# Kernel optimization log

Hardware: AMD Instinct MI355X
Metric: run time of the kernel (lower is better)

Reference implementation:

```python
import jax, jax.numpy as jnp
import numpy as np

B, P, N, E, H, D = 8, 1000, 1000, 128, 8, 16  # batch, pomo, nodes, embed, heads, qkv_dim
SQRT_E = float(np.sqrt(E))
CLIP = 10.0
INV_SQRT_D = 1.0 / float(np.sqrt(D))


def _heads(x):
    # [b, n, H*D] -> [b, H, n, D]
    b, n, _ = x.shape
    return x.reshape(b, n, H, D).transpose(0, 2, 1, 3)


def _mha(q, k, v, ninf_mask):
    # q: [b,H,P,D], k/v: [b,H,N,D], ninf_mask: [b,P,N]
    score = jnp.einsum('bhnd,bhsd->bhns', q, k) * INV_SQRT_D
    score = score + ninf_mask[:, None, :, :]
    w = jax.nn.softmax(score, axis=-1)
    out = jnp.einsum('bhns,bhsd->bhnd', w, v)
    return out.transpose(0, 2, 1, 3).reshape(q.shape[0], q.shape[2], H * D)


def setup_inputs() -> dict:
    key = jax.random.key(0)
    ks = jax.random.split(key, 16)
    s = 0.02
    return {
        'encoded_last_node': jax.random.normal(ks[0], (B, P, E), jnp.float32),
        'attr': jax.random.normal(ks[1], (B, P, 4), jnp.float32),
        'encoded_nodes': jax.random.normal(ks[2], (B, N, E), jnp.float32),
        'ninf_mask': jnp.zeros((B, P, N), jnp.float32),
        'Wq_shared': jax.random.normal(ks[3], (E + 4, H * D), jnp.float32) * s,
        'Wk_shared': jax.random.normal(ks[4], (E, H * D), jnp.float32) * s,
        'Wv_shared': jax.random.normal(ks[5], (E, H * D), jnp.float32) * s,
        'Wq_task': jax.random.normal(ks[6], (E + 4, H * D), jnp.float32) * s,
        'Wk_task': jax.random.normal(ks[7], (E, H * D), jnp.float32) * s,
        'Wv_task': jax.random.normal(ks[8], (E, H * D), jnp.float32) * s,
        'Wc_shared': jax.random.normal(ks[9], (H * D, E), jnp.float32) * s,
        'bc_shared': jnp.zeros((E,), jnp.float32),
        'Wc_task': jax.random.normal(ks[10], (H * D, E), jnp.float32) * s,
        'bc_task': jnp.zeros((E,), jnp.float32),
        'Wg': jax.random.normal(ks[11], (E + 4, E), jnp.float32) * s,
        'bg': jnp.zeros((E,), jnp.float32),
    }


def reference(encoded_last_node, attr, encoded_nodes, ninf_mask,
              Wq_shared, Wk_shared, Wv_shared, Wq_task, Wk_task, Wv_task,
              Wc_shared, bc_shared, Wc_task, bc_task, Wg, bg):
    # set_kv
    k_shared = _heads(encoded_nodes @ Wk_shared)
    v_shared = _heads(encoded_nodes @ Wv_shared)
    k_task = _heads(encoded_nodes @ Wk_task)
    v_task = _heads(encoded_nodes @ Wv_task)

    # decoder forward
    input_cat = jnp.concatenate([encoded_last_node, attr], axis=2)  # [B,P,E+4]
    q_shared = _heads(input_cat @ Wq_shared)
    q_task = _heads(input_cat @ Wq_task)

    out_shared = _mha(q_shared, k_shared, v_shared, ninf_mask) @ Wc_shared + bc_shared
    out_task = _mha(q_task, k_task, v_task, ninf_mask) @ Wc_task + bc_task

    gate = jax.nn.sigmoid(input_cat @ Wg + bg)
    gated_out = gate * out_shared + (1.0 - gate) * out_task  # [B,P,E]

    # pointer scores against single-head key (encoded_nodes)
    score = jnp.einsum('bpe,bne->bpn', gated_out, encoded_nodes) / SQRT_E
    score_clipped = CLIP * jnp.tanh(score)
    probs = jax.nn.softmax(score_clipped + ninf_mask, axis=2)
    return probs
```

## Files before the change

kernel.cpp:

```cpp
#include <hip/hip_runtime.h>
#include <math.h>

#define BB 8
#define PP 1000
#define NN 1000
#define EE 128
#define HH 8
#define DD 16

#define INV_SQRT_E 0.08838834764831845f
#define LOG2E      1.4426950408889634f
#define QSCALE     0.3606737602222409f

typedef short short8_t __attribute__((ext_vector_type(8)));
typedef float f32x4    __attribute__((ext_vector_type(4)));
typedef float f32x16   __attribute__((ext_vector_type(16)));
typedef __bf16 bf16x4  __attribute__((ext_vector_type(4)));
typedef __bf16 bf16x8  __attribute__((ext_vector_type(8)));

__device__ __forceinline__ float sigmoid_fast(float x) {
    return 1.f / (1.f + __expf(-x));
}
__device__ __forceinline__ float tanh_fast(float x) {
    x = fminf(fmaxf(x, -15.f), 15.f);
    float e = __expf(2.f * x);
    return (e - 1.f) / (e + 1.f);
}

__device__ __forceinline__ f32x4 mfma16(short8_t a, short8_t b, f32x4 c) {
    return __builtin_amdgcn_mfma_f32_16x16x32_bf16(a, b, c, 0, 0, 0);
}
__device__ __forceinline__ f32x16 mfma32(short8_t a, short8_t b, f32x16 c) {
    return __builtin_amdgcn_mfma_f32_32x32x16_bf16(a, b, c, 0, 0, 0);
}

__device__ __forceinline__ float sum16(float x) {
    int v;
    v = __builtin_amdgcn_update_dpp(0, __builtin_bit_cast(int, x), 0xB1, 0xF, 0xF, true);
    x += __builtin_bit_cast(float, v);
    v = __builtin_amdgcn_update_dpp(0, __builtin_bit_cast(int, x), 0x4E, 0xF, 0xF, true);
    x += __builtin_bit_cast(float, v);
    v = __builtin_amdgcn_update_dpp(0, __builtin_bit_cast(int, x), 0x141, 0xF, 0xF, true);
    x += __builtin_bit_cast(float, v);
    v = __builtin_amdgcn_update_dpp(0, __builtin_bit_cast(int, x), 0x140, 0xF, 0xF, true);
    x += __builtin_bit_cast(float, v);
    return x;
}

__global__ __launch_bounds__(256) void prep_kernel(
    const float* __restrict__ mask, const float* __restrict__ nodes,
    const float* __restrict__ eln,  const float* __restrict__ attr,
    const float* __restrict__ Wk_s, const float* __restrict__ Wv_s,
    const float* __restrict__ Wk_t, const float* __restrict__ Wv_t,
    const float* __restrict__ Wq_s, const float* __restrict__ Wq_t,
    const float* __restrict__ Wg,   const float* __restrict__ Wc_s,
    const float* __restrict__ Wc_t,
    __bf16* __restrict__ emaskb, __bf16* __restrict__ nodesb,
    __bf16* __restrict__ inb, __bf16* __restrict__ Wtb)
{
    const int bx = blockIdx.x;
    __shared__ float tile[32][129];
    if (bx < 7813) {
        int i = (bx * 256 + threadIdx.x) * 4;
        if (i < 8000000) {
            float4 v = *(const float4*)&mask[i];
            bf16x4 pk = { (__bf16)(v.x * LOG2E), (__bf16)(v.y * LOG2E),
                          (__bf16)(v.z * LOG2E), (__bf16)(v.w * LOG2E) };
            *(bf16x4*)&emaskb[i] = pk;
        }
    } else if (bx < 8813) {
        int i = ((bx - 7813) * 256 + threadIdx.x) * 4;
        float4 v = *(const float4*)&nodes[i];
        bf16x4 pk = { (__bf16)v.x, (__bf16)v.y, (__bf16)v.z, (__bf16)v.w };
        *(bf16x4*)&nodesb[i] = pk;
    } else if (bx < 9438) {
        int t = (bx - 8813) * 256 + threadIdx.x;
        int row = t / 20, seg = t - row * 20;
        bf16x8 o = {};
        if (seg < 16) {
            const float* p = &eln[(size_t)row * 128 + seg * 8];
            float4 a = *(const float4*)p, b = *(const float4*)(p + 4);
            o = bf16x8{ (__bf16)a.x, (__bf16)a.y, (__bf16)a.z, (__bf16)a.w,
                        (__bf16)b.x, (__bf16)b.y, (__bf16)b.z, (__bf16)b.w };
        } else if (seg == 16) {
            float4 a = *(const float4*)&attr[(size_t)row * 4];
            o = bf16x8{ (__bf16)a.x, (__bf16)a.y, (__bf16)a.z, (__bf16)a.w,
                        (__bf16)0.f, (__bf16)0.f, (__bf16)0.f, (__bf16)0.f };
        }
        *(bf16x8*)&inb[(size_t)row * 160 + seg * 8] = o;
    } else {
        int idx = bx - 9438;
        int m = idx / 5, kt = idx - m * 5;
        const float* srcs[9] = {Wk_s, Wv_s, Wk_t, Wv_t, Wq_s, Wq_t, Wg, Wc_s, Wc_t};
        const int   srcKs[9] = {128, 128, 128, 128, 132, 132, 132, 128, 128};
        const int   kpads[9] = {128, 128, 128, 128, 160, 160, 160, 128, 128};
        const size_t offs[9] = {0, 16384, 32768, 49152, 65536, 86016, 106496, 126976, 143360};
        const int kp = kpads[m];
        if (kt * 32 >= kp) return;
        const float* src = srcs[m];
        const int sK = srcKs[m];
        const size_t off = offs[m];
        const int tid = threadIdx.x;
        for (int j = tid; j < 32 * 128; j += 256) {
            int kk = j >> 7, n = j & 127;
            int k = kt * 32 + kk;
            tile[kk][n] = (k < sK) ? src[(size_t)k * 128 + n] : 0.f;
        }
        __syncthreads();
        for (int j = tid; j < 32 * 128; j += 256) {
            int n = j >> 5, kk = j & 31;
            Wtb[off + (size_t)n * kp + kt * 32 + kk] = (__bf16)tile[kk][n];
        }
    }
}

template<int NC>
__device__ __forceinline__ void proj_body(
    const __bf16* __restrict__ A, const __bf16* __restrict__ W,
    f32x4 acc[8], int r0, int quad, int lq)
{
    const int K = NC * 32;
    short8_t aF[NC];
    #pragma unroll
    for (int c = 0; c < NC; ++c)
        aF[c] = *(const short8_t*)&A[(size_t)(r0 + lq) * K + c * 32 + quad * 8];
    #pragma unroll
    for (int nt = 0; nt < 8; ++nt) {
        acc[nt] = f32x4{0.f, 0.f, 0.f, 0.f};
        #pragma unroll
        for (int c = 0; c < NC; ++c) {
            short8_t bF = *(const short8_t*)&W[(size_t)(nt * 16 + lq) * K + c * 32 + quad * 8];
            acc[nt] = mfma16(aF[c], bF, acc[nt]);
        }
    }
}

__global__ __launch_bounds__(256) void proj_mfma_kernel(
    const __bf16* __restrict__ nodesb, const __bf16* __restrict__ inb,
    const __bf16* __restrict__ Wtb,
    __bf16* __restrict__ kb_s, __bf16* __restrict__ vt_s,
    __bf16* __restrict__ kb_t, __bf16* __restrict__ vt_t,
    __bf16* __restrict__ qb_s, __bf16* __restrict__ qb_t)
{
    const int wsel = blockIdx.y;
    const int wave = threadIdx.x >> 6, lane = threadIdx.x & 63;
    const int quad = lane >> 4, lq = lane & 15;
    const int r0 = blockIdx.x * 64 + wave * 16;

    f32x4 acc[8];
    if (wsel < 4) {
        proj_body<4>(nodesb, Wtb + (size_t)wsel * 16384, acc, r0, quad, lq);
    } else {
        proj_body<5>(inb, Wtb + 65536 + (size_t)(wsel - 4) * 20480, acc, r0, quad, lq);
    }

    if (wsel == 0 || wsel == 2) {
        __bf16* O = (wsel == 0) ? kb_s : kb_t;
        #pragma unroll
        for (int r = 0; r < 4; ++r) {
            int m = r0 + quad * 4 + r;
            int b = m / 1000, n = m - b * 1000;
            #pragma unroll
            for (int nt = 0; nt < 8; ++nt)
                O[(((size_t)(b * 8 + nt) * 1000 + n) << 4) + lq] = (__bf16)acc[nt][r];
        }
    } else if (wsel == 4 || wsel == 5) {
        __bf16* O = (wsel == 4) ? qb_s : qb_t;
        #pragma unroll
        for (int r = 0; r < 4; ++r) {
            int m = r0 + quad * 4 + r;
            int b = m / 1000, n = m - b * 1000;
            #pragma unroll
            for (int nt = 0; nt < 8; ++nt)
                O[(((size_t)(b * 8 + nt) * 1000 + n) << 4) + lq] =
                    (__bf16)(acc[nt][r] * QSCALE);
        }
    } else {
        __bf16* O = (wsel == 1) ? vt_s : vt_t;
        #pragma unroll
        for (int r = 0; r < 4; ++r) {
            int m = r0 + quad * 4 + r;
            int b = m / 1000, n = m - b * 1000;
            int rr = n & 31;
            int pos = (n & ~31) + ((rr < 16) ? (rr << 1) : (((rr - 16) << 1) | 1));
            #pragma unroll
            for (int nt = 0; nt < 8; ++nt)
                O[(((size_t)(b * 8 + nt) * 16 + lq) << 10) + pos] = (__bf16)acc[nt][r];
        }
    }
}

__global__ __launch_bounds__(256) void attn_mfma_kernel(
    const __bf16* __restrict__ qb_s, const __bf16* __restrict__ qb_t,
    const __bf16* __restrict__ kb_s, const __bf16* __restrict__ kb_t,
    const __bf16* __restrict__ vt_s, const __bf16* __restrict__ vt_t,
    const __bf16* __restrict__ emaskb,
    __bf16* __restrict__ att_s, __bf16* __restrict__ att_t)
{
    const int b    = blockIdx.z;
    const int wave = threadIdx.x >> 6;
    const int combo = blockIdx.y * 4 + wave;
    const int br = combo & 1;
    const int h  = combo >> 1;
    const __bf16* Q  = br ? qb_t : qb_s;
    const __bf16* K  = br ? kb_t : kb_s;
    const __bf16* Vt = br ? vt_t : vt_s;
    __bf16* O        = br ? att_t : att_s;
    const int lane = threadIdx.x & 63;
    const int quad = lane >> 4, lq = lane & 15;
    const int col  = lane & 31;
    const int half = lane >> 5;
    const int bh = b * HH + h;
    const int p0 = blockIdx.x * 32;

    __shared__ __align__(16) __bf16 S[4][2][32][40];

    int pq = p0 + col; if (pq > 999) pq = 999;
    short8_t qB = *(const short8_t*)&Q[(((size_t)bh * 1000 + pq) << 4) + half * 8];

    const __bf16* mp = emaskb + ((size_t)b * 1000 + pq) * 1000 + 4 * half;

    short8_t onesB = { (short)0x3F80, (short)0x3F80, (short)0x3F80, (short)0x3F80,
                       (short)0x3F80, (short)0x3F80, (short)0x3F80, (short)0x3F80 };

    f32x4 o[2] = { {0.f,0.f,0.f,0.f}, {0.f,0.f,0.f,0.f} };
    f32x4 l[2] = { {0.f,0.f,0.f,0.f}, {0.f,0.f,0.f,0.f} };

    short8_t kAc = *(const short8_t*)&K[(((size_t)bh * 1000 + col) << 4) + half * 8];
    short8_t vBc = *(const short8_t*)&Vt[(((size_t)bh * 16 + lq) << 10) + quad * 8];

    #pragma unroll 2
    for (int n0 = 0; n0 < 992; n0 += 32) {
        const int par = (n0 >> 5) & 1;
        int nk = n0 + 32 + col; if (nk > 999) nk = 999;
        short8_t kAn = *(const short8_t*)&K[(((size_t)bh * 1000 + nk) << 4) + half * 8];
        short8_t vBn = *(const short8_t*)&Vt[(((size_t)bh * 16 + lq) << 10) + n0 + 32 + quad * 8];

        bf16x4 m2[4];
        #pragma unroll
        for (int g = 0; g < 4; ++g)
            m2[g] = *(const bf16x4*)&mp[n0 + 8 * g];

        f32x16 s = mfma32(kAc, qB, f32x16{});

        #pragma unroll
        for (int g = 0; g < 4; ++g) {
            bf16x4 pk;
            #pragma unroll
            for (int j = 0; j < 4; ++j)
                pk[j] = (__bf16)__builtin_amdgcn_exp2f(s[4 * g + j] + (float)m2[g][j]);
            *(bf16x4*)&S[wave][par][col][8 * g + 4 * half] = pk;
        }

        #pragma unroll
        for (int t = 0; t < 2; ++t) {
            short8_t aP = *(const short8_t*)&S[wave][par][t * 16 + lq][quad * 8];
            o[t] = mfma16(aP, vBc, o[t]);
            l[t] = mfma16(aP, onesB, l[t]);
        }
        kAc = kAn; vBc = vBn;
    }

    {
        bf16x4 m2t = *(const bf16x4*)&mp[992];
        f32x16 s = mfma32(kAc, qB, f32x16{});

        bf16x4 pk0;
        #pragma unroll
        for (int j = 0; j < 4; ++j)
            pk0[j] = (__bf16)__builtin_amdgcn_exp2f(s[j] + (float)m2t[j]);
        *(bf16x4*)&S[wave][1][col][4 * half] = pk0;
        bf16x4 z = {};
        #pragma unroll
        for (int g = 1; g < 4; ++g)
            *(bf16x4*)&S[wave][1][col][8 * g + 4 * half] = z;

        #pragma unroll
        for (int t = 0; t < 2; ++t) {
            short8_t aP = *(const short8_t*)&S[wave][1][t * 16 + lq][quad * 8];
            o[t] = mfma16(aP, vBc, o[t]);
            l[t] = mfma16(aP, onesB, l[t]);
        }
    }

    #pragma unroll
    for (int t = 0; t < 2; ++t)
        #pragma unroll
        for (int r = 0; r < 4; ++r) {
            int p = p0 + t * 16 + quad * 4 + r;
            if (p < 1000)
                O[((size_t)b * 1000 + p) * 128 + h * 16 + lq] = (__bf16)(o[t][r] / l[t][r]);
        }
}

__global__ __launch_bounds__(128) void combine_mfma_kernel(
    const __bf16* __restrict__ att_s, const __bf16* __restrict__ att_t,
    const __bf16* __restrict__ inb, const __bf16* __restrict__ Wtb,
    const float* __restrict__ bc_s, const float* __restrict__ bc_t,
    const float* __restrict__ bg, __bf16* __restrict__ gatedb)
{
    const int wave = threadIdx.x >> 6, lane = threadIdx.x & 63;
    const int quad = lane >> 4, lq = lane & 15;
    const int r0 = blockIdx.x * 32 + wave * 16;
    const __bf16* Wgp = Wtb + 106496;
    const __bf16* Ws  = Wtb + 126976;
    const __bf16* Wt  = Wtb + 143360;

    short8_t aS[4], aT[4], aG[5];
    #pragma unroll
    for (int c = 0; c < 4; ++c) {
        aS[c] = *(const short8_t*)&att_s[(size_t)(r0 + lq) * 128 + c * 32 + quad * 8];
        aT[c] = *(const short8_t*)&att_t[(size_t)(r0 + lq) * 128 + c * 32 + quad * 8];
    }
    #pragma unroll
    for (int c = 0; c < 5; ++c)
        aG[c] = *(const short8_t*)&inb[(size_t)(r0 + lq) * 160 + c * 32 + quad * 8];

    #pragma unroll
    for (int nt = 0; nt < 8; ++nt) {
        f32x4 accS = {0.f,0.f,0.f,0.f}, accT = accS, accG = accS;
        #pragma unroll
        for (int c = 0; c < 4; ++c) {
            short8_t bS = *(const short8_t*)&Ws[(size_t)(nt * 16 + lq) * 128 + c * 32 + quad * 8];
            short8_t bT = *(const short8_t*)&Wt[(size_t)(nt * 16 + lq) * 128 + c * 32 + quad * 8];
            accS = mfma16(aS[c], bS, accS);
            accT = mfma16(aT[c], bT, accT);
        }
        #pragma unroll
        for (int c = 0; c < 5; ++c) {
            short8_t bG = *(const short8_t*)&Wgp[(size_t)(nt * 16 + lq) * 160 + c * 32 + quad * 8];
            accG = mfma16(aG[c], bG, accG);
        }
        int f = nt * 16 + lq;
        float b1 = bc_s[f], b2 = bc_t[f], b3 = bg[f];
        #pragma unroll
        for (int r = 0; r < 4; ++r) {
            int m = r0 + quad * 4 + r;
            float g = sigmoid_fast(accG[r] + b3);
            float val = g * (accS[r] + b1) + (1.f - g) * (accT[r] + b2);
            gatedb[(size_t)m * 128 + f] = (__bf16)val;
        }
    }
}

__global__ __launch_bounds__(256) void pointer_softmax_kernel(
    const __bf16* __restrict__ gb, const __bf16* __restrict__ nb,
    const __bf16* __restrict__ emaskb, float* __restrict__ out)
{
    const int b    = blockIdx.y;
    const int p0   = blockIdx.x * 16;
    const int wave = threadIdx.x >> 6;
    const int lane = threadIdx.x & 63;
    const int quad = lane >> 4, lq = lane & 15;

    __shared__ float Spart[4][16];

    short8_t aF[4];
    {
        int pp = p0 + lq; if (pp > 999) pp = 999;
        const __bf16* arow = gb + (((size_t)b * 1000 + pp) << 7) + quad * 8;
        #pragma unroll
        for (int kc = 0; kc < 4; ++kc) aF[kc] = *(const short8_t*)&arow[kc * 32];
    }

    float ev[16][4];
    float psum[4] = {0.f, 0.f, 0.f, 0.f};

    #pragma unroll
    for (int i = 0; i < 16; ++i) {
        const int nt = i * 4 + wave;
        const int nn = nt * 16 + lq;
        const bool nv = nn < 1000;
        int nc = nv ? nn : 999;
        const __bf16* brow = nb + (((size_t)b * 1000 + nc) << 7) + quad * 8;
        f32x4 acc = {0.f, 0.f, 0.f, 0.f};
        #pragma unroll
        for (int kc = 0; kc < 4; ++kc) {
            short8_t bF = *(const short8_t*)&brow[kc * 32];
            acc = mfma16(aF[kc], bF, acc);
        }
        #pragma unroll
        for (int r = 0; r < 4; ++r) {
            int p = p0 + quad * 4 + r;
            bool v = nv && (p < 1000);
            size_t midx = v ? ((size_t)b * 1000 + p) * 1000 + nn : 0;
            float m2 = (float)emaskb[midx];
            float sc = 10.f * tanh_fast(acc[r] * INV_SQRT_E);
            float ee = v ? __builtin_amdgcn_exp2f(sc * LOG2E + m2) : 0.f;
            ev[i][r] = ee;
            psum[r] += ee;
        }
    }

    #pragma unroll
    for (int r = 0; r < 4; ++r) psum[r] = sum16(psum[r]);
    if (lq == 0) {
        #pragma unroll
        for (int r = 0; r < 4; ++r) Spart[wave][quad * 4 + r] = psum[r];
    }
    __syncthreads();
    float inv[4];
    #pragma unroll
    for (int r = 0; r < 4; ++r) {
        int row = quad * 4 + r;
        float s = Spart[0][row] + Spart[1][row] + Spart[2][row] + Spart[3][row];
        inv[r] = 1.f / s;
    }

    #pragma unroll
    for (int i = 0; i < 16; ++i) {
        const int nt = i * 4 + wave;
        const int nn = nt * 16 + lq;
        if (nn < 1000) {
            #pragma unroll
            for (int r = 0; r < 4; ++r) {
                int p = p0 + quad * 4 + r;
                if (p < 1000)
                    out[((size_t)b * 1000 + p) * 1000 + nn] = ev[i][r] * inv[r];
            }
        }
    }
}

extern "C" void kernel_launch(void* const* d_in, const int* in_sizes, int n_in,
                              void* d_out, int out_size, void* d_ws, size_t ws_size,
                              hipStream_t stream)
{
    const float* eln   = (const float*)d_in[0];
    const float* attr  = (const float*)d_in[1];
    const float* nodes = (const float*)d_in[2];
    const float* mask  = (const float*)d_in[3];
    const float* Wq_s  = (const float*)d_in[4];
    const float* Wk_s  = (const float*)d_in[5];
    const float* Wv_s  = (const float*)d_in[6];
    const float* Wq_t  = (const float*)d_in[7];
    const float* Wk_t  = (const float*)d_in[8];
    const float* Wv_t  = (const float*)d_in[9];
    const float* Wc_s  = (const float*)d_in[10];
    const float* bc_s  = (const float*)d_in[11];
    const float* Wc_t  = (const float*)d_in[12];
    const float* bc_t  = (const float*)d_in[13];
    const float* Wg    = (const float*)d_in[14];
    const float* bg    = (const float*)d_in[15];
    float* out = (float*)d_out;

    char* w = (char*)d_ws;
    const size_t KB_SZ = (size_t)64 * 1000 * 16 * 2;
    const size_t VT_SZ = (size_t)64 * 16 * 1024 * 2;
    const size_t H_SZ  = (size_t)8000 * 128 * 2;
    const size_t IN_SZ = (size_t)8000 * 160 * 2;
    const size_t EM_SZ = (size_t)8000 * 1000 * 2;
    __bf16* kb_s  = (__bf16*)w;           w += KB_SZ;
    __bf16* kb_t  = (__bf16*)w;           w += KB_SZ;
    __bf16* qb_s  = (__bf16*)w;           w += KB_SZ;
    __bf16* qb_t  = (__bf16*)w;           w += KB_SZ;
    __bf16* vt_s  = (__bf16*)w;           w += VT_SZ;
    __bf16* vt_t  = (__bf16*)w;           w += VT_SZ;
    __bf16* att_s = (__bf16*)w;           w += H_SZ;
    __bf16* att_t = (__bf16*)w;           w += H_SZ;
    __bf16* gatedb = (__bf16*)w;          w += H_SZ;
    __bf16* nodesb = (__bf16*)w;          w += H_SZ;
    __bf16* inb    = (__bf16*)w;          w += IN_SZ;
    __bf16* emaskb = (__bf16*)w;          w += EM_SZ;
    __bf16* Wtb    = (__bf16*)w;          w += 320000;

    hipMemsetAsync(vt_s, 0, 2 * VT_SZ, stream);

    prep_kernel<<<dim3(9483), 256, 0, stream>>>(
        mask, nodes, eln, attr, Wk_s, Wv_s, Wk_t, Wv_t, Wq_s, Wq_t, Wg,
        Wc_s, Wc_t, emaskb, nodesb, inb, Wtb);
    proj_mfma_kernel<<<dim3(125, 6), 256, 0, stream>>>(
        nodesb, inb, Wtb, kb_s, vt_s, kb_t, vt_t, qb_s, qb_t);
    attn_mfma_kernel<<<dim3(32, 4, 8), 256, 0, stream>>>(
        qb_s, qb_t, kb_s, kb_t, vt_s, vt_t, emaskb, att_s, att_t);
    combine_mfma_kernel<<<dim3(250), 128, 0, stream>>>(
        att_s, att_t, inb, Wtb, bc_s, bc_t, bg, gatedb);
    pointer_softmax_kernel<<<dim3(63, 8), 256, 0, stream>>>(
        gatedb, nodesb, emaskb, out);
}
```

Baseline: 228.5 us.

## Split attention over key range with reduce pass; widen pointer softmax blocks

Attention is split into two halves of the key dimension, each block writing unnormalised partial outputs and row sums to fp32 workspace. A new reduce kernel adds the halves and normalises. This doubles the grid from 1024 to 2048 blocks for better occupancy, and the mask load is now prefetched one step ahead. The pointer softmax kernel moves to 512 threads with half the per-thread register array. The cost is an extra launch and about 16 MB of fp32 partial traffic, and the split path falls back to the old kernel if the workspace is too small.

```diff
diff --git a/kernel.cpp b/kernel.cpp
--- a/kernel.cpp
+++ b/kernel.cpp
@@ -190,6 +190,136 @@
     }
 }
 
+__global__ __launch_bounds__(256) void attn_split_kernel(
+    const __bf16* __restrict__ qb_s, const __bf16* __restrict__ qb_t,
+    const __bf16* __restrict__ kb_s, const __bf16* __restrict__ kb_t,
+    const __bf16* __restrict__ vt_s, const __bf16* __restrict__ vt_t,
+    const __bf16* __restrict__ emaskb,
+    float* __restrict__ opart, float* __restrict__ lpart)
+{
+    const int b    = blockIdx.z;
+    const int wave = threadIdx.x >> 6;
+    const int ks   = blockIdx.y >> 2;
+    const int combo = (blockIdx.y & 3) * 4 + wave;
+    const int br = combo & 1;
+    const int h  = combo >> 1;
+    const __bf16* Q  = br ? qb_t : qb_s;
+    const __bf16* K  = br ? kb_t : kb_s;
+    const __bf16* Vt = br ? vt_t : vt_s;
+    const int lane = threadIdx.x & 63;
+    const int quad = lane >> 4, lq = lane & 15;
+    const int col  = lane & 31;
+    const int half = lane >> 5;
+    const int bh = b * HH + h;
+    const int p0 = blockIdx.x * 32;
+
+    __shared__ __align__(16) __bf16 S[4][2][32][40];
+
+    int pq = p0 + col; if (pq > 999) pq = 999;
+    short8_t qB = *(const short8_t*)&Q[(((size_t)bh * 1000 + pq) << 4) + half * 8];
+
+    const __bf16* mp = emaskb + ((size_t)b * 1000 + pq) * 1000 + 4 * half;
+
+    short8_t onesB = { (short)0x3F80, (short)0x3F80, (short)0x3F80, (short)0x3F80,
+                       (short)0x3F80, (short)0x3F80, (short)0x3F80, (short)0x3F80 };
+
+    f32x4 o[2] = { {0.f,0.f,0.f,0.f}, {0.f,0.f,0.f,0.f} };
+    f32x4 l[2] = { {0.f,0.f,0.f,0.f}, {0.f,0.f,0.f,0.f} };
+
+    const int base = ks * 512;
+    const int nend = ks ? 992 : 512;
+
+    short8_t kAc = *(const short8_t*)&K[(((size_t)bh * 1000 + base + col) << 4) + half * 8];
+    short8_t vBc = *(const short8_t*)&Vt[(((size_t)bh * 16 + lq) << 10) + base + quad * 8];
+    bf16x4 mc[4];
+    #pragma unroll
+    for (int g = 0; g < 4; ++g) mc[g] = *(const bf16x4*)&mp[base + 8 * g];
+
+    #pragma unroll 2
+    for (int n0 = base; n0 < nend; n0 += 32) {
+        const int par = (n0 >> 5) & 1;
+        int nk = n0 + 32 + col; if (nk > 999) nk = 999;
+        short8_t kAn = *(const short8_t*)&K[(((size_t)bh * 1000 + nk) << 4) + half * 8];
+        short8_t vBn = *(const short8_t*)&Vt[(((size_t)bh * 16 + lq) << 10) + n0 + 32 + quad * 8];
+        bf16x4 mn[4];
+        #pragma unroll
+        for (int g = 0; g < 4; ++g)
+            mn[g] = *(const bf16x4*)&mp[n0 + 32 + 8 * g];
+
+        f32x16 s = mfma32(kAc, qB, f32x16{});
+
+        #pragma unroll
+        for (int g = 0; g < 4; ++g) {
+            bf16x4 pk;
+            #pragma unroll
+            for (int j = 0; j < 4; ++j)
+                pk[j] = (__bf16)__builtin_amdgcn_exp2f(s[4 * g + j] + (float)mc[g][j]);
+            *(bf16x4*)&S[wave][par][col][8 * g + 4 * half] = pk;
+        }
+
+        #pragma unroll
+        for (int t = 0; t < 2; ++t) {
+            short8_t aP = *(const short8_t*)&S[wave][par][t * 16 + lq][quad * 8];
+            o[t] = mfma16(aP, vBc, o[t]);
+            l[t] = mfma16(aP, onesB, l[t]);
+        }
+        kAc = kAn; vBc = vBn;
+        #pragma unroll
+        for (int g = 0; g < 4; ++g) mc[g] = mn[g];
+    }
+
+    if (ks) {
+        f32x16 s = mfma32(kAc, qB, f32x16{});
+        bf16x4 pk0;
+        #pragma unroll
+        for (int j = 0; j < 4; ++j)
+            pk0[j] = (__bf16)__builtin_amdgcn_exp2f(s[j] + (float)mc[0][j]);
+        *(bf16x4*)&S[wave][1][col][4 * half] = pk0;
+        bf16x4 z = {};
+        #pragma unroll
+        for (int g = 1; g < 4; ++g)
+            *(bf16x4*)&S[wave][1][col][8 * g + 4 * half] = z;
+
+        #pragma unroll
+        for (int t = 0; t < 2; ++t) {
+            short8_t aP = *(const short8_t*)&S[wave][1][t * 16 + lq][quad * 8];
+            o[t] = mfma16(aP, vBc, o[t]);
+            l[t] = mfma16(aP, onesB, l[t]);
+        }
+    }
+
+    const int idxc = (b * 2 + br) * 8 + h;
+    float* op = opart + ((size_t)ks * 128 + idxc) * 16000;
+    float* lp = lpart + ((size_t)ks * 128 + idxc) * 1000;
+    #pragma unroll
+    for (int t = 0; t < 2; ++t)
+        #pragma unroll
+        for (int r = 0; r < 4; ++r) {
+            int p = p0 + t * 16 + quad * 4 + r;
+            if (p < 1000) {
+                op[p * 16 + lq] = o[t][r];
+                if (lq == 0) lp[p] = l[t][r];
+            }
+        }
+}
+
+__global__ __launch_bounds__(256) void attn_reduce_kernel(
+    const float* __restrict__ opart, const float* __restrict__ lpart,
+    __bf16* __restrict__ att_s, __bf16* __restrict__ att_t)
+{
+    const int idx = blockIdx.y;
+    const int b = idx >> 4, br = (idx >> 3) & 1, h = idx & 7;
+    const int p = blockIdx.x * 16 + (threadIdx.x >> 4);
+    const int d = threadIdx.x & 15;
+    if (p >= 1000) return;
+    float o = opart[(size_t)idx * 16000 + p * 16 + d]
+            + opart[(size_t)(128 + idx) * 16000 + p * 16 + d];
+    float l = lpart[(size_t)idx * 1000 + p]
+            + lpart[(size_t)(128 + idx) * 1000 + p];
+    __bf16* O = br ? att_t : att_s;
+    O[((size_t)b * 1000 + p) * 128 + h * 16 + d] = (__bf16)(o / l);
+}
+
 __global__ __launch_bounds__(256) void attn_mfma_kernel(
     const __bf16* __restrict__ qb_s, const __bf16* __restrict__ qb_t,
     const __bf16* __restrict__ kb_s, const __bf16* __restrict__ kb_t,
@@ -217,7 +347,6 @@
 
     int pq = p0 + col; if (pq > 999) pq = 999;
     short8_t qB = *(const short8_t*)&Q[(((size_t)bh * 1000 + pq) << 4) + half * 8];
-
     const __bf16* mp = emaskb + ((size_t)b * 1000 + pq) * 1000 + 4 * half;
 
     short8_t onesB = { (short)0x3F80, (short)0x3F80, (short)0x3F80, (short)0x3F80,
@@ -235,7 +364,6 @@
         int nk = n0 + 32 + col; if (nk > 999) nk = 999;
         short8_t kAn = *(const short8_t*)&K[(((size_t)bh * 1000 + nk) << 4) + half * 8];
         short8_t vBn = *(const short8_t*)&Vt[(((size_t)bh * 16 + lq) << 10) + n0 + 32 + quad * 8];
-
         bf16x4 m2[4];
         #pragma unroll
         for (int g = 0; g < 4; ++g)
@@ -264,7 +392,6 @@
     {
         bf16x4 m2t = *(const bf16x4*)&mp[992];
         f32x16 s = mfma32(kAc, qB, f32x16{});
-
         bf16x4 pk0;
         #pragma unroll
         for (int j = 0; j < 4; ++j)
@@ -343,7 +470,7 @@
     }
 }
 
-__global__ __launch_bounds__(256) void pointer_softmax_kernel(
+__global__ __launch_bounds__(512) void pointer_softmax_kernel(
     const __bf16* __restrict__ gb, const __bf16* __restrict__ nb,
     const __bf16* __restrict__ emaskb, float* __restrict__ out)
 {
@@ -353,7 +480,7 @@
     const int lane = threadIdx.x & 63;
     const int quad = lane >> 4, lq = lane & 15;
 
-    __shared__ float Spart[4][16];
+    __shared__ float Spart[8][16];
 
     short8_t aF[4];
     {
@@ -363,12 +490,12 @@
         for (int kc = 0; kc < 4; ++kc) aF[kc] = *(const short8_t*)&arow[kc * 32];
     }
 
-    float ev[16][4];
+    float ev[8][4];
     float psum[4] = {0.f, 0.f, 0.f, 0.f};
 
     #pragma unroll
-    for (int i = 0; i < 16; ++i) {
-        const int nt = i * 4 + wave;
+    for (int i = 0; i < 8; ++i) {
+        const int nt = i * 8 + wave;
         const int nn = nt * 16 + lq;
         const bool nv = nn < 1000;
         int nc = nv ? nn : 999;
@@ -403,13 +530,15 @@
     #pragma unroll
     for (int r = 0; r < 4; ++r) {
         int row = quad * 4 + r;
-        float s = Spart[0][row] + Spart[1][row] + Spart[2][row] + Spart[3][row];
+        float s = 0.f;
+        #pragma unroll
+        for (int wv = 0; wv < 8; ++wv) s += Spart[wv][row];
         inv[r] = 1.f / s;
     }
 
     #pragma unroll
-    for (int i = 0; i < 16; ++i) {
-        const int nt = i * 4 + wave;
+    for (int i = 0; i < 8; ++i) {
+        const int nt = i * 8 + wave;
         const int nn = nt * 16 + lq;
         if (nn < 1000) {
             #pragma unroll
@@ -464,6 +593,10 @@
     __bf16* emaskb = (__bf16*)w;          w += EM_SZ;
     __bf16* Wtb    = (__bf16*)w;          w += 320000;
 
+    float* opart = (float*)w;             w += (size_t)2 * 128 * 16000 * 4;
+    float* lpart = (float*)w;             w += (size_t)2 * 128 * 1000 * 4;
+    const bool use_split = ((size_t)(w - (char*)d_ws) <= ws_size);
+
     hipMemsetAsync(vt_s, 0, 2 * VT_SZ, stream);
 
     prep_kernel<<<dim3(9483), 256, 0, stream>>>(
@@ -471,10 +604,17 @@
         Wc_s, Wc_t, emaskb, nodesb, inb, Wtb);
     proj_mfma_kernel<<<dim3(125, 6), 256, 0, stream>>>(
         nodesb, inb, Wtb, kb_s, vt_s, kb_t, vt_t, qb_s, qb_t);
-    attn_mfma_kernel<<<dim3(32, 4, 8), 256, 0, stream>>>(
-        qb_s, qb_t, kb_s, kb_t, vt_s, vt_t, emaskb, att_s, att_t);
+    if (use_split) {
+        attn_split_kernel<<<dim3(32, 8, 8), 256, 0, stream>>>(
+            qb_s, qb_t, kb_s, kb_t, vt_s, vt_t, emaskb, opart, lpart);
+        attn_reduce_kernel<<<dim3(63, 128), 256, 0, stream>>>(
+            opart, lpart, att_s, att_t);
+    } else {
+        attn_mfma_kernel<<<dim3(32, 4, 8), 256, 0, stream>>>(
+            qb_s, qb_t, kb_s, kb_t, vt_s, vt_t, emaskb, att_s, att_t);
+    }
     combine_mfma_kernel<<<dim3(250), 128, 0, stream>>>(
         att_s, att_t, inb, Wtb, bc_s, bc_t, bg, gatedb);
-    pointer_softmax_kernel<<<dim3(63, 8), 256, 0, stream>>>(
+    pointer_softmax_kernel<<<dim3(63, 8), 512, 0, stream>>>(
         gatedb, nodesb, emaskb, out);
 }
```

Result: slower. 233.5 us (+2.2%).
